# Kernel optimization log

Hardware: AMD Instinct MI355X
Metric: run time of the kernel (lower is better)

Reference implementation:

```python
import jax, jax.numpy as jnp
import numpy as np

NEG = -1e9  # masked_fill value from the original
B, S, E, H, L, V, CTX = 4, 1024, 1024, 16, 12, 50257, 1024
D = E // H
PAD_IDX = 0


def layernorm(x, g, b, eps=1e-5):
    m = jnp.mean(x, axis=-1, keepdims=True)
    v = jnp.var(x, axis=-1, keepdims=True)
    return (x - m) * jax.lax.rsqrt(v + eps) * g + b


def setup_inputs() -> dict:
    key = jax.random.key(0)
    ks = jax.random.split(key, 8)
    sc = 0.02
    init = lambda k, shape: (jax.random.normal(k, shape, jnp.float32) * sc)
    return {
        "x": jax.random.randint(ks[0], (B, S), 0, V),
        "wte": init(ks[1], (V, E)),
        "wpe": init(ks[2], (CTX, E)),
        "Wq": init(ks[3], (L, E, E)), "bq": jnp.zeros((L, E), jnp.float32),
        "Wkv": init(ks[4], (L, E, E)), "bkv": jnp.zeros((L, E), jnp.float32),
        "Wfc": init(ks[5], (L, E, 4 * E)), "bfc": jnp.zeros((L, 4 * E), jnp.float32),
        "Wproj": init(ks[6], (L, 4 * E, E)), "bproj": jnp.zeros((L, E), jnp.float32),
        "ln1_g": jnp.ones((L, E), jnp.float32), "ln1_b": jnp.zeros((L, E), jnp.float32),
        "ln2_g": jnp.ones((L, E), jnp.float32), "ln2_b": jnp.zeros((L, E), jnp.float32),
        "lnf_g": jnp.ones((E,), jnp.float32), "lnf_b": jnp.zeros((E,), jnp.float32),
    }


def reference(x, wte, wpe, Wq, bq, Wkv, bkv, Wfc, bfc, Wproj, bproj,
              ln1_g, ln1_b, ln2_g, ln2_b, lnf_g, lnf_b):
    # key padding mask: mask = (x != pad_idx) broadcast over queries
    key_mask = (x != PAD_IDX)  # (B, S) over key positions
    h = wte[x] + wpe[:S]       # (B, S, E); dropout is identity in eval

    def block(h, p):
        wq, bq_, wkv, bkv_, wfc, bfc_, wpj, bpj, g1, b1, g2, b2 = p
        # Q = c_attn(x); K = V = c_proj(x)  (shared key/value tensor, as in source)
        q = (h @ wq + bq_).reshape(B, S, H, D)
        kv = (h @ wkv + bkv_).reshape(B, S, H, D)
        # unscaled QK^T (original applies no 1/sqrt(d) scaling)
        scores = jnp.einsum('blhd,bmhd->bhlm', q, kv)          # (B,H,S,S)
        scores = jnp.where(key_mask[:, None, None, :], scores, NEG)
        probs = jax.nn.softmax(scores, axis=-1)                # attn dropout = identity
        attn = jnp.einsum('bhlm,bmhd->blhd', probs, kv).reshape(B, S, E)
        u = layernorm(h + attn, g1, b1)                        # ln_1(x + attn)
        m = jax.nn.gelu(u @ wfc + bfc_, approximate=False) @ wpj + bpj
        # NOTE: second residual is the BLOCK INPUT h (not u), per the source
        return layernorm(m + h, g2, b2), None

    h, _ = jax.lax.scan(
        block, h,
        (Wq, bq, Wkv, bkv, Wfc, bfc, Wproj, bproj, ln1_g, ln1_b, ln2_g, ln2_b))
    return layernorm(h, lnf_g, lnf_b)
```

## Files before the change

kernel.cpp:

```cpp
#include <hip/hip_runtime.h>

#define SEQ    1024
#define EDIM   1024
#define NHEAD  16
#define DHEAD  64
#define NLAYER 12
#define NTOK   4096
#define QKVN   2048

typedef float f32x4  __attribute__((ext_vector_type(4)));
typedef short bf16x8 __attribute__((ext_vector_type(8)));

__device__ __forceinline__ unsigned short f32_to_bf16(float f) {
    union { float f; unsigned u; } v; v.f = f;
    return (unsigned short)((v.u + 0x7fffu + ((v.u >> 16) & 1u)) >> 16);
}

__device__ __forceinline__ void gload_lds16(const unsigned short* g, unsigned short* l) {
    __builtin_amdgcn_global_load_lds((const __attribute__((address_space(1))) void*)g,
                                     (__attribute__((address_space(3))) void*)l, 16, 0, 0);
}

#define BARRIER() do { __builtin_amdgcn_s_barrier(); asm volatile("" ::: "memory"); } while (0)

__global__ __launch_bounds__(256) void transpose_bf16_k(
    const float* __restrict__ W, unsigned short* __restrict__ WT,
    int K, int N, size_t wStride, size_t wtStride)
{
    __shared__ float tile[32][33];
    const int l = blockIdx.z;
    W  += (size_t)l * wStride;
    WT += (size_t)l * wtStride;
    const int n0 = blockIdx.x * 32, k0 = blockIdx.y * 32;
    const int t = threadIdx.x;
    const int r = t >> 3, c4 = (t & 7) * 4;
    const float4 v = *reinterpret_cast<const float4*>(&W[(size_t)(k0 + r) * N + n0 + c4]);
    tile[r][c4 + 0] = v.x; tile[r][c4 + 1] = v.y;
    tile[r][c4 + 2] = v.z; tile[r][c4 + 3] = v.w;
    __syncthreads();
    ushort4 o;
    o.x = f32_to_bf16(tile[c4 + 0][r]);
    o.y = f32_to_bf16(tile[c4 + 1][r]);
    o.z = f32_to_bf16(tile[c4 + 2][r]);
    o.w = f32_to_bf16(tile[c4 + 3][r]);
    *reinterpret_cast<ushort4*>(&WT[(size_t)(n0 + r) * K + k0 + c4]) = o;
}

__global__ __launch_bounds__(256) void bias_concat_k(
    const float* __restrict__ bq, const float* __restrict__ bkv,
    float* __restrict__ bqkv)
{
    const int l = blockIdx.x, t = threadIdx.x;
    #pragma unroll
    for (int i = 0; i < 4; ++i) {
        const int c = t + i * 256;
        bqkv[(size_t)l * QKVN + c]        = bq[(size_t)l * EDIM + c];
        bqkv[(size_t)l * QKVN + EDIM + c] = bkv[(size_t)l * EDIM + c];
    }
}

__global__ __launch_bounds__(256) void embed_k(
    const int* __restrict__ x, const float* __restrict__ wte,
    const float* __restrict__ wpe, float* __restrict__ h,
    unsigned short* __restrict__ hb)
{
    const int bs  = blockIdx.x;
    const int s   = bs & (SEQ - 1);
    const int tok = x[bs];
    const int c   = threadIdx.x * 4;
    float4 a = *reinterpret_cast<const float4*>(&wte[(size_t)tok * EDIM + c]);
    const float4 p = *reinterpret_cast<const float4*>(&wpe[(size_t)s * EDIM + c]);
    a.x += p.x; a.y += p.y; a.z += p.z; a.w += p.w;
    *reinterpret_cast<float4*>(&h[(size_t)bs * EDIM + c]) = a;
    ushort4 o;
    o.x = f32_to_bf16(a.x); o.y = f32_to_bf16(a.y);
    o.z = f32_to_bf16(a.z); o.w = f32_to_bf16(a.w);
    *reinterpret_cast<ushort4*>(&hb[(size_t)bs * EDIM + c]) = o;
}

template<int NADD, int WF32, int WBF16>
__global__ __launch_bounds__(256) void add_ln_k(
    const float* __restrict__ x1, const float* __restrict__ x2,
    const float* __restrict__ x3, const float* __restrict__ g,
    const float* __restrict__ b, float* __restrict__ outf,
    unsigned short* __restrict__ outb)
{
    const int row = blockIdx.x;
    const int t   = threadIdx.x;
    const int c   = t * 4;
    const size_t base = (size_t)row * EDIM + c;
    float4 a = *reinterpret_cast<const float4*>(x1 + base);
    if (NADD >= 2) {
        const float4 v = *reinterpret_cast<const float4*>(x2 + base);
        a.x += v.x; a.y += v.y; a.z += v.z; a.w += v.w;
    }
    if (NADD >= 3) {
        const float4 v = *reinterpret_cast<const float4*>(x3 + base);
        a.x += v.x; a.y += v.y; a.z += v.z; a.w += v.w;
    }
    float s  = a.x + a.y + a.z + a.w;
    float ss = a.x * a.x + a.y * a.y + a.z * a.z + a.w * a.w;
    #pragma unroll
    for (int o = 32; o > 0; o >>= 1) {
        s  += __shfl_down(s, o);
        ss += __shfl_down(ss, o);
    }
    __shared__ float rs[4], rss[4];
    const int lane = t & 63, wv = t >> 6;
    if (lane == 0) { rs[wv] = s; rss[wv] = ss; }
    __syncthreads();
    s  = rs[0] + rs[1] + rs[2] + rs[3];
    ss = rss[0] + rss[1] + rss[2] + rss[3];
    const float mean = s * (1.f / EDIM);
    const float var  = ss * (1.f / EDIM) - mean * mean;
    const float inv  = rsqrtf(var + 1e-5f);
    const float4 gv = *reinterpret_cast<const float4*>(g + c);
    const float4 bv = *reinterpret_cast<const float4*>(b + c);
    float4 y;
    y.x = (a.x - mean) * inv * gv.x + bv.x;
    y.y = (a.y - mean) * inv * gv.y + bv.y;
    y.z = (a.z - mean) * inv * gv.z + bv.z;
    y.w = (a.w - mean) * inv * gv.w + bv.w;
    if (WF32) *reinterpret_cast<float4*>(outf + base) = y;
    if (WBF16) {
        ushort4 o;
        o.x = f32_to_bf16(y.x); o.y = f32_to_bf16(y.y);
        o.z = f32_to_bf16(y.z); o.w = f32_to_bf16(y.w);
        *reinterpret_cast<ushort4*>(outb + base) = o;
    }
}

template<int GELU, int OUTBF16>
__global__ __launch_bounds__(256) void gemm_bt_k(
    const unsigned short* __restrict__ A,
    const unsigned short* __restrict__ BT,
    const float* __restrict__ bias, void* __restrict__ Cout,
    void* __restrict__ Cout2, int M, int N, int K)
{
    __shared__ unsigned short As[128 * 32];
    __shared__ unsigned short Bs[128 * 32];

    const int t    = threadIdx.x;
    const int lane = t & 63;
    const int wave = t >> 6;
    const int wr   = wave >> 1, wc = wave & 1;
    const int lrow = lane & 15, lgrp = lane >> 4;

    const int nbx = gridDim.x;
    int flat = blockIdx.y * nbx + blockIdx.x;
    const int nwg = nbx * gridDim.y;
    flat = (flat & 7) * (nwg >> 3) + (flat >> 3);
    const int row0 = (flat / nbx) * 128, col0 = (flat % nbx) * 128;

    const int kspan = K / gridDim.z;
    const int koff  = blockIdx.z * kspan;

    const int srow  = lane >> 2;
    const int skoff = (lane & 3) * 8;
    const unsigned short* aP0 = A  + (size_t)(row0 + 32 * wave + srow) * K + skoff;
    const unsigned short* aP1 = aP0 + (size_t)16 * K;
    const unsigned short* bP0 = BT + (size_t)(col0 + 32 * wave + srow) * K + skoff;
    const unsigned short* bP1 = bP0 + (size_t)16 * K;
    unsigned short* aL0 = As + wave * 1024;
    unsigned short* aL1 = As + wave * 1024 + 512;
    unsigned short* bL0 = Bs + wave * 1024;
    unsigned short* bL1 = Bs + wave * 1024 + 512;

    f32x4 acc[4][4];
    #pragma unroll
    for (int i = 0; i < 4; ++i)
        #pragma unroll
        for (int j = 0; j < 4; ++j)
            acc[i][j] = (f32x4){0.f, 0.f, 0.f, 0.f};

    for (int k0 = koff; k0 < koff + kspan; k0 += 32) {
        gload_lds16(aP0 + k0, aL0);
        gload_lds16(aP1 + k0, aL1);
        gload_lds16(bP0 + k0, bL0);
        gload_lds16(bP1 + k0, bL1);
        __syncthreads();

        bf16x8 af[4], bf[4];
        #pragma unroll
        for (int m = 0; m < 4; ++m)
            af[m] = *reinterpret_cast<const bf16x8*>(
                &As[(wr * 64 + m * 16 + lrow) * 32 + lgrp * 8]);
        #pragma unroll
        for (int n = 0; n < 4; ++n)
            bf[n] = *reinterpret_cast<const bf16x8*>(
                &Bs[(wc * 64 + n * 16 + lrow) * 32 + lgrp * 8]);

        #pragma unroll
        for (int n = 0; n < 4; ++n)
            #pragma unroll
            for (int m = 0; m < 4; ++m)
                acc[m][n] = __builtin_amdgcn_mfma_f32_16x16x32_bf16(
                    af[m], bf[n], acc[m][n], 0, 0, 0);
        __syncthreads();
    }

    const int z = blockIdx.z;
    #pragma unroll
    for (int n = 0; n < 4; ++n) {
        const int col = col0 + wc * 64 + n * 16 + lrow;
        const float bv = (z == 0) ? bias[col] : 0.f;
        #pragma unroll
        for (int m = 0; m < 4; ++m) {
            const int rb = row0 + wr * 64 + m * 16 + lgrp * 4;
            #pragma unroll
            for (int r = 0; r < 4; ++r) {
                float xv = acc[m][n][r] + bv;
                if (GELU) xv = 0.5f * xv * (1.f + erff(xv * 0.70710678118654752f));
                if (OUTBF16) {
                    ((unsigned short*)Cout)[(size_t)(rb + r) * N + col] = f32_to_bf16(xv);
                } else {
                    float* dst = (z == 0) ? (float*)Cout : (float*)Cout2;
                    dst[(size_t)(rb + r) * N + col] = xv;
                }
            }
        }
    }
}

template<int GELU>
__global__ __launch_bounds__(512) void gemm256_k(
    const unsigned short* __restrict__ A,
    const unsigned short* __restrict__ BT,
    const float* __restrict__ bias, unsigned short* __restrict__ C,
    int M, int N, int K)
{
    __shared__ unsigned short sh[65536];
    unsigned short* Asm = sh;
    unsigned short* Bsm = sh + 32768;

    const int tid  = threadIdx.x;
    const int lane = tid & 63;
    const int wave = tid >> 6;
    const int wm   = wave >> 2;
    const int wn   = wave & 3;
    const int lrow = lane & 15, lgrp = lane >> 4;

    const int ntc = N >> 8;
    const int nwg = gridDim.x;
    int flat = (blockIdx.x & 7) * (nwg >> 3) + (blockIdx.x >> 3);
    const int row0 = (flat / ntc) * 256;
    const int col0 = (flat % ntc) * 256;
    const int NT = K >> 6;

    f32x4 acc[8][4];
    #pragma unroll
    for (int i = 0; i < 8; ++i)
        #pragma unroll
        for (int j = 0; j < 4; ++j)
            acc[i][j] = (f32x4){0.f, 0.f, 0.f, 0.f};

    auto stage_half = [&](const unsigned short* g, unsigned short* l) {
        #pragma unroll
        for (int c = 0; c < 2; ++c) {
            const int d = (tid + c * 512) * 16;
            const int L = d ^ (((d >> 7) & 7) << 4);
            gload_lds16(g + (size_t)(L >> 7) * K + ((L & 127) >> 1), l + (d >> 1));
        }
    };
    auto stageA = [&](int buf, int kt, int h) {
        stage_half(A + (size_t)(row0 + h * 128) * K + kt * 64,
                   Asm + buf * 16384 + h * 8192);
    };
    auto stageB = [&](int buf, int kt, int h) {
        stage_half(BT + (size_t)(col0 + h * 128) * K + kt * 64,
                   Bsm + buf * 16384 + h * 8192);
    };

    auto rdA = [&](int buf, int p, bf16x8 (&af)[2][2]) {
        #pragma unroll
        for (int m = 0; m < 2; ++m)
            #pragma unroll
            for (int ks = 0; ks < 2; ++ks) {
                const int r  = wm * 128 + p * 32 + m * 16 + lrow;
                const int cB = (ks * 64 + lgrp * 16) ^ ((r & 7) << 4);
                af[m][ks] = *reinterpret_cast<const bf16x8*>(
                    &Asm[buf * 16384 + ((r * 128 + cB) >> 1)]);
            }
    };
    auto rdB = [&](int buf, bf16x8 (&bfr)[4][2]) {
        #pragma unroll
        for (int n = 0; n < 4; ++n)
            #pragma unroll
            for (int ks = 0; ks < 2; ++ks) {
                const int r  = wn * 64 + n * 16 + lrow;
                const int cB = (ks * 64 + lgrp * 16) ^ ((r & 7) << 4);
                bfr[n][ks] = *reinterpret_cast<const bf16x8*>(
                    &Bsm[buf * 16384 + ((r * 128 + cB) >> 1)]);
            }
    };
    auto mq = [&](int p, bf16x8 (&af)[2][2], bf16x8 (&bfr)[4][2]) {
        __builtin_amdgcn_s_setprio(1);
        #pragma unroll
        for (int ks = 0; ks < 2; ++ks)
            #pragma unroll
            for (int n = 0; n < 4; ++n)
                #pragma unroll
                for (int m = 0; m < 2; ++m)
                    acc[p * 2 + m][n] = __builtin_amdgcn_mfma_f32_16x16x32_bf16(
                        af[m][ks], bfr[n][ks], acc[p * 2 + m][n], 0, 0, 0);
        __builtin_amdgcn_s_setprio(0);
    };

    stageA(0, 0, 0); stageA(0, 0, 1);
    stageB(0, 0, 0); stageB(0, 0, 1);
    stageA(1, 1, 0); stageA(1, 1, 1);
    stageB(1, 1, 0); stageB(1, 1, 1);
    asm volatile("s_waitcnt vmcnt(8)" ::: "memory");
    BARRIER();

    for (int t = 0; t < NT; t += 2) {
        bf16x8 bfr[4][2], af[2][2];
        rdB(0, bfr); rdA(0, 0, af);
        if (t > 0) { stageA(1, t + 1, 0); stageA(1, t + 1, 1); }
        BARRIER(); mq(0, af, bfr); BARRIER();
        rdA(0, 1, af);
        if (t + 2 < NT) stageB(0, t + 2, 0);
        BARRIER(); mq(1, af, bfr); BARRIER();
        rdA(0, 2, af);
        if (t + 2 < NT) stageB(0, t + 2, 1);
        BARRIER(); mq(2, af, bfr); BARRIER();
        rdA(0, 3, af);
        BARRIER(); mq(3, af, bfr);
        if (t + 2 < NT) { asm volatile("s_waitcnt vmcnt(4)" ::: "memory"); }
        else            { asm volatile("s_waitcnt vmcnt(0)" ::: "memory"); }
        BARRIER();
        rdB(1, bfr); rdA(1, 0, af);
        if (t + 2 < NT) stageA(0, t + 2, 0);
        BARRIER(); mq(0, af, bfr); BARRIER();
        rdA(1, 1, af);
        if (t + 2 < NT) stageA(0, t + 2, 1);
        if (t + 3 < NT) stageB(1, t + 3, 0);
        BARRIER(); mq(1, af, bfr); BARRIER();
        rdA(1, 2, af);
        if (t + 3 < NT) stageB(1, t + 3, 1);
        BARRIER(); mq(2, af, bfr); BARRIER();
        rdA(1, 3, af);
        BARRIER(); mq(3, af, bfr);
        if (t + 2 < NT) { asm volatile("s_waitcnt vmcnt(4)" ::: "memory"); }
        BARRIER();
    }

    #pragma unroll
    for (int n = 0; n < 4; ++n) {
        const int col = col0 + wn * 64 + n * 16 + lrow;
        const float bv = bias[col];
        #pragma unroll
        for (int mf = 0; mf < 8; ++mf) {
            const int rb = row0 + wm * 128 + mf * 16 + lgrp * 4;
            #pragma unroll
            for (int r = 0; r < 4; ++r) {
                float xv = acc[mf][n][r] + bv;
                if (GELU) xv = 0.5f * xv * (1.f + erff(xv * 0.70710678118654752f));
                C[(size_t)(rb + r) * N + col] = f32_to_bf16(xv);
            }
        }
    }
}

#define KVP 68
__global__ __launch_bounds__(256) void attn_k(
    const unsigned short* __restrict__ qkv, const int* __restrict__ x,
    float* __restrict__ out)
{
    __shared__ unsigned short KVr[64][KVP];
    __shared__ unsigned short KVt[64 * 64];
    __shared__ unsigned short Ps[4][32][KVP];
    __shared__ float maskf[64];

    int flat = blockIdx.x + 8 * (blockIdx.y + 16 * blockIdx.z);
    flat = (flat & 7) * 64 + (flat >> 3);
    const int qt = flat & 7;
    const int hh = (flat >> 3) & 15;
    const int b  = flat >> 7;

    const int t    = threadIdx.x;
    const int w    = t >> 6;
    const int lane = t & 63;
    const int lrow = lane & 15, lgrp = lane >> 4;

    const unsigned short* qb_  = qkv + ((size_t)b * SEQ) * QKVN + hh * DHEAD;
    const unsigned short* kvb_ = qkv + ((size_t)b * SEQ) * QKVN + EDIM + hh * DHEAD;
    const int* xb = x + b * SEQ;
    const int qrow0 = qt * 128 + w * 32;

    bf16x8 qf[2][2];
    #pragma unroll
    for (int m = 0; m < 2; ++m)
        #pragma unroll
        for (int ks = 0; ks < 2; ++ks)
            qf[m][ks] = *reinterpret_cast<const bf16x8*>(
                qb_ + (size_t)(qrow0 + m * 16 + lrow) * QKVN + ks * 32 + lgrp * 8);

    f32x4 O[2][4];
    float mrun[2][4], lrun[2][4];
    #pragma unroll
    for (int m = 0; m < 2; ++m)
        #pragma unroll
        for (int i = 0; i < 4; ++i) {
            O[m][i] = (f32x4){0.f, 0.f, 0.f, 0.f};
            mrun[m][i] = -3e30f; lrun[m][i] = 0.f;
        }

    for (int kt = 0; kt < SEQ / 64; ++kt) {
        __syncthreads();
        #pragma unroll
        for (int i = 0; i < 4; ++i) {
            const int u2 = t + i * 256;
            const int kr = u2 >> 4, kc = (u2 & 15) * 4;
            const ushort4 v = *reinterpret_cast<const ushort4*>(
                &kvb_[(size_t)(kt * 64 + kr) * QKVN + kc]);
            *reinterpret_cast<ushort4*>(&KVr[kr][kc]) = v;
            const unsigned short comp[4] = {v.x, v.y, v.z, v.w};
            #pragma unroll
            for (int j = 0; j < 4; ++j) {
                const int d = kc + j;
                const int sw = (d ^ (d >> 3)) & 7;
                KVt[(d * 128 + ((kr * 2) ^ (sw << 4))) >> 1] = comp[j];
            }
        }
        if (t < 64) maskf[t] = (xb[kt * 64 + t] != 0) ? 1.f : 0.f;
        __syncthreads();

        f32x4 s[2][4];
        #pragma unroll
        for (int m = 0; m < 2; ++m)
            #pragma unroll
            for (int n = 0; n < 4; ++n) s[m][n] = (f32x4){0.f, 0.f, 0.f, 0.f};
        #pragma unroll
        for (int ks = 0; ks < 2; ++ks)
            #pragma unroll
            for (int n = 0; n < 4; ++n) {
                union { bf16x8 v; ushort4 h[2]; } bb;
                bb.h[0] = *reinterpret_cast<const ushort4*>(
                    &KVr[16 * n + lrow][ks * 32 + lgrp * 8]);
                bb.h[1] = *reinterpret_cast<const ushort4*>(
                    &KVr[16 * n + lrow][ks * 32 + lgrp * 8 + 4]);
                #pragma unroll
                for (int m = 0; m < 2; ++m)
                    s[m][n] = __builtin_amdgcn_mfma_f32_16x16x32_bf16(
                        qf[m][ks], bb.v, s[m][n], 0, 0, 0);
            }

        #pragma unroll
        for (int n = 0; n < 4; ++n) {
            const float flag = maskf[16 * n + lrow];
            #pragma unroll
            for (int m = 0; m < 2; ++m)
                #pragma unroll
                for (int r = 0; r < 4; ++r)
                    s[m][n][r] = (flag != 0.f) ? s[m][n][r] : -1e9f;
        }

        #pragma unroll
        for (int m = 0; m < 2; ++m)
            #pragma unroll
            for (int r = 0; r < 4; ++r) {
                float v = fmaxf(fmaxf(s[m][0][r], s[m][1][r]),
                                fmaxf(s[m][2][r], s[m][3][r]));
                #pragma unroll
                for (int o = 1; o < 16; o <<= 1) v = fmaxf(v, __shfl_xor(v, o));
                const float mn = fmaxf(mrun[m][r], v);
                const float fs = __expf(mrun[m][r] - mn);
                mrun[m][r] = mn;
                lrun[m][r] *= fs;
                #pragma unroll
                for (int df = 0; df < 4; ++df) O[m][df][r] *= fs;
            }

        #pragma unroll
        for (int m = 0; m < 2; ++m) {
            float rsum[4] = {0.f, 0.f, 0.f, 0.f};
            #pragma unroll
            for (int n = 0; n < 4; ++n)
                #pragma unroll
                for (int r = 0; r < 4; ++r) {
                    const float p = __expf(s[m][n][r] - mrun[m][r]);
                    rsum[r] += p;
                    Ps[w][m * 16 + 4 * lgrp + r][16 * n + lrow] = f32_to_bf16(p);
                }
            #pragma unroll
            for (int r = 0; r < 4; ++r) {
                float v = rsum[r];
                #pragma unroll
                for (int o = 1; o < 16; o <<= 1) v += __shfl_xor(v, o);
                lrun[m][r] += v;
            }
        }

        #pragma unroll
        for (int ks = 0; ks < 2; ++ks) {
            bf16x8 paf[2];
            #pragma unroll
            for (int m = 0; m < 2; ++m) {
                union { bf16x8 v; ushort4 h[2]; } pp;
                pp.h[0] = *reinterpret_cast<const ushort4*>(
                    &Ps[w][m * 16 + lrow][ks * 32 + lgrp * 8]);
                pp.h[1] = *reinterpret_cast<const ushort4*>(
                    &Ps[w][m * 16 + lrow][ks * 32 + lgrp * 8 + 4]);
                paf[m] = pp.v;
            }
            #pragma unroll
            for (int df = 0; df < 4; ++df) {
                const int d  = 16 * df + lrow;
                const int sw = (d ^ (d >> 3)) & 7;
                const bf16x8 bvf = *reinterpret_cast<const bf16x8*>(
                    &KVt[(d * 128 + ((ks * 64 + lgrp * 16) ^ (sw << 4))) >> 1]);
                #pragma unroll
                for (int m = 0; m < 2; ++m)
                    O[m][df] = __builtin_amdgcn_mfma_f32_16x16x32_bf16(
                        paf[m], bvf, O[m][df], 0, 0, 0);
            }
        }
    }

    #pragma unroll
    for (int m = 0; m < 2; ++m)
        #pragma unroll
        for (int r = 0; r < 4; ++r) {
            const float inv = 1.f / lrun[m][r];
            const int row = qrow0 + m * 16 + 4 * lgrp + r;
            float* po = out + ((size_t)b * SEQ + row) * EDIM + hh * DHEAD;
            #pragma unroll
            for (int df = 0; df < 4; ++df)
                po[16 * df + lrow] = O[m][df][r] * inv;
        }
}

extern "C" void kernel_launch(void* const* d_in, const int* in_sizes, int n_in,
                              void* d_out, int out_size, void* d_ws, size_t ws_size,
                              hipStream_t stream)
{
    (void)in_sizes; (void)n_in; (void)out_size; (void)ws_size;

    const int*   x     = (const int*)  d_in[0];
    const float* wte   = (const float*)d_in[1];
    const float* wpe   = (const float*)d_in[2];
    const float* Wq    = (const float*)d_in[3];
    const float* bq    = (const float*)d_in[4];
    const float* Wkv   = (const float*)d_in[5];
    const float* bkv   = (const float*)d_in[6];
    const float* Wfc   = (const float*)d_in[7];
    const float* bfc   = (const float*)d_in[8];
    const float* Wproj = (const float*)d_in[9];
    const float* bproj = (const float*)d_in[10];
    const float* ln1g  = (const float*)d_in[11];
    const float* ln1b  = (const float*)d_in[12];
    const float* ln2g  = (const float*)d_in[13];
    const float* ln2b  = (const float*)d_in[14];
    const float* lnfg  = (const float*)d_in[15];
    const float* lnfb  = (const float*)d_in[16];

    const size_t MB = 1024 * 1024;
    char* W = (char*)d_ws;
    float*          h     = (float*)(W + 0 * MB);
    float*          att   = (float*)(W + 16 * MB);
    float*          mb    = (float*)(W + 32 * MB);
    unsigned short* hb    = (unsigned short*)(W + 48 * MB);
    unsigned short* qkv   = (unsigned short*)(W + 56 * MB);
    unsigned short* ub    = (unsigned short*)(W + 72 * MB);
    unsigned short* tb    = (unsigned short*)(W + 80 * MB);
    float*          bqkv  = (float*)(W + 112 * MB);
    unsigned short* wqkvT = (unsigned short*)(W + 113 * MB);
    unsigned short* wfcT  = (unsigned short*)(W + 161 * MB);
    unsigned short* wpjT  = (unsigned short*)(W + 257 * MB);

    bias_concat_k<<<NLAYER, 256, 0, stream>>>(bq, bkv, bqkv);
    transpose_bf16_k<<<dim3(32, 32, NLAYER), 256, 0, stream>>>(
        Wq, wqkvT, EDIM, EDIM, (size_t)EDIM * EDIM, (size_t)QKVN * EDIM);
    transpose_bf16_k<<<dim3(32, 32, NLAYER), 256, 0, stream>>>(
        Wkv, wqkvT + (size_t)EDIM * EDIM, EDIM, EDIM,
        (size_t)EDIM * EDIM, (size_t)QKVN * EDIM);
    transpose_bf16_k<<<dim3(128, 32, NLAYER), 256, 0, stream>>>(
        Wfc, wfcT, EDIM, 4 * EDIM, (size_t)4 * EDIM * EDIM, (size_t)4 * EDIM * EDIM);
    transpose_bf16_k<<<dim3(32, 128, NLAYER), 256, 0, stream>>>(
        Wproj, wpjT, 4 * EDIM, EDIM, (size_t)4 * EDIM * EDIM, (size_t)4 * EDIM * EDIM);

    embed_k<<<NTOK, 256, 0, stream>>>(x, wte, wpe, h, hb);

    for (int l = 0; l < NLAYER; ++l) {
        gemm_bt_k<0, 1><<<dim3(QKVN / 128, NTOK / 128), 256, 0, stream>>>(
            hb, wqkvT + (size_t)l * QKVN * EDIM, bqkv + (size_t)l * QKVN,
            qkv, nullptr, NTOK, QKVN, EDIM);

        attn_k<<<dim3(SEQ / 128, NHEAD, 4), 256, 0, stream>>>(qkv, x, att);

        add_ln_k<2, 0, 1><<<NTOK, 256, 0, stream>>>(
            h, att, nullptr, ln1g + l * EDIM, ln1b + l * EDIM, nullptr, ub);

        gemm256_k<1><<<dim3((NTOK / 256) * (4 * EDIM / 256)), 512, 0, stream>>>(
            ub, wfcT + (size_t)l * 4 * EDIM * EDIM, bfc + (size_t)l * 4 * EDIM,
            tb, NTOK, 4 * EDIM, EDIM);

        gemm_bt_k<0, 0><<<dim3(EDIM / 128, NTOK / 128, 2), 256, 0, stream>>>(
            tb, wpjT + (size_t)l * 4 * EDIM * EDIM, bproj + (size_t)l * EDIM,
            mb, att, NTOK, EDIM, 4 * EDIM);

        add_ln_k<3, 1, 1><<<NTOK, 256, 0, stream>>>(
            mb, att, h, ln2g + l * EDIM, ln2b + l * EDIM, h, hb);
    }

    add_ln_k<1, 1, 0><<<NTOK, 256, 0, stream>>>(
        h, nullptr, nullptr, lnfg, lnfb, (float*)d_out, nullptr);
}
```

Baseline: 2.952 ms.

## Use 256-tile split-K=4 GEMM for MLP projection and prefetch attention KV tiles

The MLP down-projection (K=4096, N=1024) moves from the 128-tile gemm with split-K=2 to the 256x256 gemm256 kernel with split-K=4. Four fp32 partials are written and summed in an extended 5-input add+layernorm kernel. The attention kernel now loads the next KV tile and mask values into registers before computing on the current tile, to hide global load latency. The split path runs only when the workspace is large enough, and it adds fp32 partial traffic plus register pressure in attention.

```diff
diff --git a/kernel.cpp b/kernel.cpp
--- a/kernel.cpp
+++ b/kernel.cpp
@@ -81,7 +81,8 @@
 template<int NADD, int WF32, int WBF16>
 __global__ __launch_bounds__(256) void add_ln_k(
     const float* __restrict__ x1, const float* __restrict__ x2,
-    const float* __restrict__ x3, const float* __restrict__ g,
+    const float* __restrict__ x3, const float* __restrict__ x4,
+    const float* __restrict__ x5, const float* __restrict__ g,
     const float* __restrict__ b, float* __restrict__ outf,
     unsigned short* __restrict__ outb)
 {
@@ -96,6 +97,14 @@
     }
     if (NADD >= 3) {
         const float4 v = *reinterpret_cast<const float4*>(x3 + base);
+        a.x += v.x; a.y += v.y; a.z += v.z; a.w += v.w;
+    }
+    if (NADD >= 4) {
+        const float4 v = *reinterpret_cast<const float4*>(x4 + base);
+        a.x += v.x; a.y += v.y; a.z += v.z; a.w += v.w;
+    }
+    if (NADD >= 5) {
+        const float4 v = *reinterpret_cast<const float4*>(x5 + base);
         a.x += v.x; a.y += v.y; a.z += v.z; a.w += v.w;
     }
     float s  = a.x + a.y + a.z + a.w;
@@ -222,11 +231,13 @@
     }
 }
 
-template<int GELU>
+template<int GELU, int OUT>
 __global__ __launch_bounds__(512) void gemm256_k(
     const unsigned short* __restrict__ A,
     const unsigned short* __restrict__ BT,
     const float* __restrict__ bias, unsigned short* __restrict__ C,
+    float* __restrict__ P0, float* __restrict__ P1,
+    float* __restrict__ P2, float* __restrict__ P3,
     int M, int N, int K)
 {
     __shared__ unsigned short sh[65536];
@@ -245,7 +256,10 @@
     int flat = (blockIdx.x & 7) * (nwg >> 3) + (blockIdx.x >> 3);
     const int row0 = (flat / ntc) * 256;
     const int col0 = (flat % ntc) * 256;
-    const int NT = K >> 6;
+
+    const int kspan = K / gridDim.y;
+    const int koff  = blockIdx.y * kspan;
+    const int NT    = kspan >> 6;
 
     f32x4 acc[8][4];
     #pragma unroll
@@ -263,11 +277,11 @@
         }
     };
     auto stageA = [&](int buf, int kt, int h) {
-        stage_half(A + (size_t)(row0 + h * 128) * K + kt * 64,
+        stage_half(A + (size_t)(row0 + h * 128) * K + koff + kt * 64,
                    Asm + buf * 16384 + h * 8192);
     };
     auto stageB = [&](int buf, int kt, int h) {
-        stage_half(BT + (size_t)(col0 + h * 128) * K + kt * 64,
+        stage_half(BT + (size_t)(col0 + h * 128) * K + koff + kt * 64,
                    Bsm + buf * 16384 + h * 8192);
     };
 
@@ -345,10 +359,11 @@
         BARRIER();
     }
 
+    const int z = blockIdx.y;
     #pragma unroll
     for (int n = 0; n < 4; ++n) {
         const int col = col0 + wn * 64 + n * 16 + lrow;
-        const float bv = bias[col];
+        const float bv = (z == 0) ? bias[col] : 0.f;
         #pragma unroll
         for (int mf = 0; mf < 8; ++mf) {
             const int rb = row0 + wm * 128 + mf * 16 + lgrp * 4;
@@ -356,7 +371,12 @@
             for (int r = 0; r < 4; ++r) {
                 float xv = acc[mf][n][r] + bv;
                 if (GELU) xv = 0.5f * xv * (1.f + erff(xv * 0.70710678118654752f));
-                C[(size_t)(rb + r) * N + col] = f32_to_bf16(xv);
+                if (OUT == 0) {
+                    C[(size_t)(rb + r) * N + col] = f32_to_bf16(xv);
+                } else {
+                    float* dst = (z == 0) ? P0 : (z == 1) ? P1 : (z == 2) ? P2 : P3;
+                    dst[(size_t)(rb + r) * N + col] = xv;
+                }
             }
         }
     }
@@ -406,16 +426,30 @@
             mrun[m][i] = -3e30f; lrun[m][i] = 0.f;
         }
 
-    for (int kt = 0; kt < SEQ / 64; ++kt) {
-        __syncthreads();
+    const int NKT = SEQ / 64;
+    ushort4 kvreg[4];
+    int xv = 0;
+
+    auto issueKV = [&](int kt) {
         #pragma unroll
         for (int i = 0; i < 4; ++i) {
             const int u2 = t + i * 256;
             const int kr = u2 >> 4, kc = (u2 & 15) * 4;
-            const ushort4 v = *reinterpret_cast<const ushort4*>(
+            kvreg[i] = *reinterpret_cast<const ushort4*>(
                 &kvb_[(size_t)(kt * 64 + kr) * QKVN + kc]);
-            *reinterpret_cast<ushort4*>(&KVr[kr][kc]) = v;
-            const unsigned short comp[4] = {v.x, v.y, v.z, v.w};
+        }
+        if (t < 64) xv = xb[kt * 64 + t];
+    };
+    issueKV(0);
+
+    for (int kt = 0; kt < NKT; ++kt) {
+        __syncthreads();
+        #pragma unroll
+        for (int i = 0; i < 4; ++i) {
+            const int u2 = t + i * 256;
+            const int kr = u2 >> 4, kc = (u2 & 15) * 4;
+            *reinterpret_cast<ushort4*>(&KVr[kr][kc]) = kvreg[i];
+            const unsigned short comp[4] = {kvreg[i].x, kvreg[i].y, kvreg[i].z, kvreg[i].w};
             #pragma unroll
             for (int j = 0; j < 4; ++j) {
                 const int d = kc + j;
@@ -423,7 +457,8 @@
                 KVt[(d * 128 + ((kr * 2) ^ (sw << 4))) >> 1] = comp[j];
             }
         }
-        if (t < 64) maskf[t] = (xb[kt * 64 + t] != 0) ? 1.f : 0.f;
+        if (t < 64) maskf[t] = (xv != 0) ? 1.f : 0.f;
+        if (kt + 1 < NKT) issueKV(kt + 1);
         __syncthreads();
 
         f32x4 s[2][4];
@@ -535,7 +570,7 @@
                               void* d_out, int out_size, void* d_ws, size_t ws_size,
                               hipStream_t stream)
 {
-    (void)in_sizes; (void)n_in; (void)out_size; (void)ws_size;
+    (void)in_sizes; (void)n_in; (void)out_size;
 
     const int*   x     = (const int*)  d_in[0];
     const float* wte   = (const float*)d_in[1];
@@ -568,6 +603,10 @@
     unsigned short* wqkvT = (unsigned short*)(W + 113 * MB);
     unsigned short* wfcT  = (unsigned short*)(W + 161 * MB);
     unsigned short* wpjT  = (unsigned short*)(W + 257 * MB);
+    float*          p2f   = (float*)(W + 56 * MB);
+    float*          p3f   = (float*)(W + 353 * MB);
+
+    const bool split4 = ws_size >= (size_t)369 * MB;
 
     bias_concat_k<<<NLAYER, 256, 0, stream>>>(bq, bkv, bqkv);
     transpose_bf16_k<<<dim3(32, 32, NLAYER), 256, 0, stream>>>(
@@ -590,20 +629,30 @@
         attn_k<<<dim3(SEQ / 128, NHEAD, 4), 256, 0, stream>>>(qkv, x, att);
 
         add_ln_k<2, 0, 1><<<NTOK, 256, 0, stream>>>(
-            h, att, nullptr, ln1g + l * EDIM, ln1b + l * EDIM, nullptr, ub);
-
-        gemm256_k<1><<<dim3((NTOK / 256) * (4 * EDIM / 256)), 512, 0, stream>>>(
+            h, att, nullptr, nullptr, nullptr,
+            ln1g + l * EDIM, ln1b + l * EDIM, nullptr, ub);
+
+        gemm256_k<1, 0><<<dim3((NTOK / 256) * (4 * EDIM / 256), 1), 512, 0, stream>>>(
             ub, wfcT + (size_t)l * 4 * EDIM * EDIM, bfc + (size_t)l * 4 * EDIM,
-            tb, NTOK, 4 * EDIM, EDIM);
-
-        gemm_bt_k<0, 0><<<dim3(EDIM / 128, NTOK / 128, 2), 256, 0, stream>>>(
-            tb, wpjT + (size_t)l * 4 * EDIM * EDIM, bproj + (size_t)l * EDIM,
-            mb, att, NTOK, EDIM, 4 * EDIM);
-
-        add_ln_k<3, 1, 1><<<NTOK, 256, 0, stream>>>(
-            mb, att, h, ln2g + l * EDIM, ln2b + l * EDIM, h, hb);
+            tb, nullptr, nullptr, nullptr, nullptr, NTOK, 4 * EDIM, EDIM);
+
+        if (split4) {
+            gemm256_k<0, 1><<<dim3((NTOK / 256) * (EDIM / 256), 4), 512, 0, stream>>>(
+                tb, wpjT + (size_t)l * 4 * EDIM * EDIM, bproj + (size_t)l * EDIM,
+                nullptr, mb, att, p2f, p3f, NTOK, EDIM, 4 * EDIM);
+            add_ln_k<5, 1, 1><<<NTOK, 256, 0, stream>>>(
+                mb, att, p2f, p3f, h,
+                ln2g + l * EDIM, ln2b + l * EDIM, h, hb);
+        } else {
+            gemm_bt_k<0, 0><<<dim3(EDIM / 128, NTOK / 128, 2), 256, 0, stream>>>(
+                tb, wpjT + (size_t)l * 4 * EDIM * EDIM, bproj + (size_t)l * EDIM,
+                mb, att, NTOK, EDIM, 4 * EDIM);
+            add_ln_k<3, 1, 1><<<NTOK, 256, 0, stream>>>(
+                mb, att, h, nullptr, nullptr,
+                ln2g + l * EDIM, ln2b + l * EDIM, h, hb);
+        }
     }
 
     add_ln_k<1, 1, 0><<<NTOK, 256, 0, stream>>>(
-        h, nullptr, nullptr, lnfg, lnfb, (float*)d_out, nullptr);
-}
+        h, nullptr, nullptr, nullptr, nullptr, lnfg, lnfb, (float*)d_out, nullptr);
+}
```

Result: faster. 2.691 ms (-8.8%).
